# Kernel optimization log

Hardware: AMD Instinct MI355X
Metric: run time of the kernel (lower is better)

The kernel has to match this reference:

```python
import jax, jax.numpy as jnp
import numpy as np

N = 100000        # nodes
E_RAND = 1500000  # random edges (self loops appended -> E = 1.6M)
IN_DIM = 500
HID = 256
NCLASS = 50
K = 10


def setup_inputs() -> dict:
    key = jax.random.key(0)
    ks = jax.random.split(key, 8)
    feats = jax.random.normal(ks[0], (N, IN_DIM), dtype=jnp.float32)
    # edges: random + self loops (fit() adds self loops)
    src_r = jax.random.randint(ks[1], (E_RAND,), 0, N, dtype=jnp.int32)
    dst_r = jax.random.randint(ks[2], (E_RAND,), 0, N, dtype=jnp.int32)
    loop = jnp.arange(N, dtype=jnp.int32)
    src = jnp.concatenate([src_r, loop])
    dst = jnp.concatenate([dst_r, loop])
    # params (xavier-uniform-like scales)
    def xavier(k, shape):
        lim = np.sqrt(6.0 / (shape[0] + shape[1]))
        return jax.random.uniform(k, shape, jnp.float32, -lim, lim)
    W1 = xavier(ks[3], (IN_DIM, HID))
    b1 = jnp.zeros((HID,), jnp.float32)
    W2 = xavier(ks[4], (HID, NCLASS))
    b2 = jnp.zeros((NCLASS,), jnp.float32)
    s = xavier(ks[5], (NCLASS, 1))
    return {"feats": feats, "W1": W1, "b1": b1, "W2": W2, "b2": b2,
            "s": s, "src": src, "dst": dst}


def reference(feats, W1, b1, W2, b2, s, src, dst):
    # --- MLP (dropout is identity in eval / p=0) ---
    x = jax.nn.relu(feats @ W1 + b1)          # [N, HID]
    x = x @ W2 + b2                            # [N, NCLASS]
    # --- DAGNNConv: k-hop sym-normalized propagation ---
    deg = jax.ops.segment_sum(jnp.ones_like(dst, dtype=jnp.float32), dst,
                              num_segments=N)  # in-degrees
    norm = jnp.power(deg, -0.5)[:, None]       # [N, 1]
    results = [x]
    h = x
    for _ in range(K):
        h = h * norm
        h = jax.ops.segment_sum(h[src], dst, num_segments=N)  # copy_u + sum
        h = h * norm
        results.append(h)
    H = jnp.stack(results, axis=1)             # [N, K+1, C]
    S = jax.nn.sigmoid(jnp.einsum('nkc,co->nk', H, s))  # [N, K+1]
    out = jnp.einsum('nk,nkc->nc', S, H)       # [N, C]
    return out
```

## Files before the change

### kernel.cpp

```cpp
#include <hip/hip_runtime.h>
#include <hip/hip_bf16.h>
#include <math.h>

#define NN     100000
#define INDIM  500
#define HID    256
#define NCLASS 50
#define KHOPS  10
#define KPAD   512
#define CPAD   64

static inline size_t roundup256(size_t x) { return (x + 255) & ~(size_t)255; }

typedef __attribute__((ext_vector_type(8))) short bf16x8;
typedef __attribute__((ext_vector_type(4))) float f32x4;
typedef __attribute__((ext_vector_type(4))) short short4v;

__device__ inline short f2bf(float f) {
    union { float f; unsigned u; } v; v.f = f;
    unsigned r = v.u + 0x7FFFu + ((v.u >> 16) & 1u);
    return (short)(r >> 16);
}
__device__ inline float bflo(unsigned u) {
    union { unsigned u; float f; } v; v.u = u << 16; return v.f;
}
__device__ inline float bfhi(unsigned u) {
    union { unsigned u; float f; } v; v.u = u & 0xFFFF0000u; return v.f;
}
__device__ inline unsigned packbf(float a, float b) {
    return (unsigned)(unsigned short)f2bf(a) | ((unsigned)(unsigned short)f2bf(b) << 16);
}

__global__ void dagnn_zero2(int* __restrict__ a, int* __restrict__ b, int n) {
    int i = blockIdx.x * blockDim.x + threadIdx.x;
    if (i < n) { a[i] = 0; b[i] = 0; }
}

__global__ void dagnn_deg(const int* __restrict__ dst, int* __restrict__ degi, int E) {
    int e = blockIdx.x * blockDim.x + threadIdx.x;
    if (e < E) atomicAdd(&degi[dst[e]], 1);
}

__global__ void dagnn_norm(const int* __restrict__ degi, float* __restrict__ nrm, int n) {
    int i = blockIdx.x * blockDim.x + threadIdx.x;
    if (i < n) nrm[i] = rsqrtf((float)degi[i]);
}

__global__ void dagnn_scan(const int* __restrict__ degi, int* __restrict__ rowptr, int n) {
    __shared__ int wsum[16];
    __shared__ int carry_s;
    const int tid  = threadIdx.x;
    const int lane = tid & 63;
    const int wid  = tid >> 6;
    if (tid == 0) carry_s = 0;
    __syncthreads();
    for (int base = 0; base < n; base += 4096) {
        int i0 = base + tid * 4;
        int v0 = (i0 + 0 < n) ? degi[i0 + 0] : 0;
        int v1 = (i0 + 1 < n) ? degi[i0 + 1] : 0;
        int v2 = (i0 + 2 < n) ? degi[i0 + 2] : 0;
        int v3 = (i0 + 3 < n) ? degi[i0 + 3] : 0;
        int tsum = v0 + v1 + v2 + v3;
        int x = tsum;
        #pragma unroll
        for (int off = 1; off < 64; off <<= 1) {
            int t = __shfl_up(x, off);
            if (lane >= off) x += t;
        }
        if (lane == 63) wsum[wid] = x;
        __syncthreads();
        if (tid == 0) {
            int run = carry_s;
            #pragma unroll
            for (int w = 0; w < 16; ++w) { int t = wsum[w]; wsum[w] = run; run += t; }
            carry_s = run;
        }
        __syncthreads();
        int texcl = wsum[wid] + (x - tsum);
        if (i0 + 0 < n) rowptr[i0 + 0] = texcl;
        if (i0 + 1 < n) rowptr[i0 + 1] = texcl + v0;
        if (i0 + 2 < n) rowptr[i0 + 2] = texcl + v0 + v1;
        if (i0 + 3 < n) rowptr[i0 + 3] = texcl + v0 + v1 + v2;
        __syncthreads();
    }
    if (tid == 0) rowptr[n] = carry_s;
}

__global__ void dagnn_fill(const int* __restrict__ src, const int* __restrict__ dst,
                           const int* __restrict__ rowptr, int* __restrict__ fillc,
                           int* __restrict__ colidx, int E) {
    int e = blockIdx.x * blockDim.x + threadIdx.x;
    if (e >= E) return;
    int d = dst[e];
    int pos = rowptr[d] + atomicAdd(&fillc[d], 1);
    colidx[pos] = src[e];
}

__global__ void dagnn_w1t(const float* __restrict__ W1, short* __restrict__ W1t) {
    int idx = blockIdx.x * 256 + threadIdx.x;
    if (idx >= HID * KPAD) return;
    int n = idx >> 9;
    int k = idx & (KPAD - 1);
    float v = (k < INDIM) ? W1[(size_t)k * HID + n] : 0.f;
    W1t[idx] = f2bf(v);
}

__global__ void dagnn_w2t(const float* __restrict__ W2, short* __restrict__ W2t) {
    int idx = blockIdx.x * 256 + threadIdx.x;
    if (idx >= CPAD * HID) return;
    int n = idx >> 8;
    int k = idx & 255;
    float v = (n < NCLASS) ? W2[(size_t)k * NCLASS + n] : 0.f;
    W2t[idx] = f2bf(v);
}

__global__ void dagnn_sgate(const float* __restrict__ svec, float2* __restrict__ sg) {
    int c = threadIdx.x;
    if (c < 32) {
        float x = (2 * c     < NCLASS) ? svec[2 * c]     : 0.f;
        float y = (2 * c + 1 < NCLASS) ? svec[2 * c + 1] : 0.f;
        sg[c] = make_float2(x, y);
    }
}

#define G1_STRIDE 40
__global__ __launch_bounds__(512) void dagnn_gemm1_mfma(
        const float* __restrict__ A, const short* __restrict__ Bt,
        const float* __restrict__ bias, short* __restrict__ C, int M) {
    __shared__ __align__(16) short As[128 * G1_STRIDE];
    __shared__ __align__(16) short Bs[256 * G1_STRIDE];

    const int tid  = threadIdx.x;
    const int lane = tid & 63;
    const int wid  = tid >> 6;
    const int l16  = lane & 15;
    const int quad = lane >> 4;
    const int m_off = (wid & 1) * 64;
    const int n_off = (wid >> 1) * 64;
    const int row0  = blockIdx.x * 128;

    int am[2], aseg[2], bn[2], bseg[2];
    #pragma unroll
    for (int it = 0; it < 2; ++it) {
        int slot = tid + it * 512;
        am[it] = slot >> 3; aseg[it] = slot & 7;
        bn[it] = slot >> 2; bseg[it] = slot & 3;
    }

    float4 ra[2]; bf16x8 rb[2];

    #define LOAD_TILE(k0)                                                     \
        _Pragma("unroll")                                                     \
        for (int it = 0; it < 2; ++it) {                                      \
            int gm = row0 + am[it];                                           \
            int gk = (k0) + aseg[it] * 4;                                     \
            float4 f = {0.f, 0.f, 0.f, 0.f};                                  \
            if (gm < M) {                                                     \
                const float* ap = A + (size_t)gm * INDIM + gk;                \
                if (gk + 3 < INDIM) f = *(const float4*)ap;                   \
                else {                                                        \
                    if (gk + 0 < INDIM) f.x = ap[0];                          \
                    if (gk + 1 < INDIM) f.y = ap[1];                          \
                    if (gk + 2 < INDIM) f.z = ap[2];                          \
                    if (gk + 3 < INDIM) f.w = ap[3];                          \
                }                                                             \
            }                                                                 \
            ra[it] = f;                                                       \
            rb[it] = *(const bf16x8*)(Bt + (size_t)bn[it] * KPAD + (k0) + bseg[it] * 8); \
        }

    #define STORE_TILE()                                                      \
        _Pragma("unroll")                                                     \
        for (int it = 0; it < 2; ++it) {                                      \
            short4v sv;                                                       \
            sv.x = f2bf(ra[it].x); sv.y = f2bf(ra[it].y);                     \
            sv.z = f2bf(ra[it].z); sv.w = f2bf(ra[it].w);                     \
            *(short4v*)&As[am[it] * G1_STRIDE + aseg[it] * 4] = sv;           \
            *(bf16x8*)&Bs[bn[it] * G1_STRIDE + bseg[it] * 8] = rb[it];        \
        }

    f32x4 acc[4][4] = {};

    LOAD_TILE(0)
    STORE_TILE()
    __syncthreads();

    for (int ks = 0; ks < KPAD / 32; ++ks) {
        if (ks + 1 < KPAD / 32) { LOAD_TILE((ks + 1) * 32) }

        bf16x8 af[4], bfr[4];
        #pragma unroll
        for (int mt = 0; mt < 4; ++mt)
            af[mt] = *(const bf16x8*)&As[(m_off + mt * 16 + l16) * G1_STRIDE + quad * 8];
        #pragma unroll
        for (int nt = 0; nt < 4; ++nt)
            bfr[nt] = *(const bf16x8*)&Bs[(n_off + nt * 16 + l16) * G1_STRIDE + quad * 8];
        #pragma unroll
        for (int mt = 0; mt < 4; ++mt)
            #pragma unroll
            for (int nt = 0; nt < 4; ++nt)
                acc[mt][nt] = __builtin_amdgcn_mfma_f32_16x16x32_bf16(
                                  af[mt], bfr[nt], acc[mt][nt], 0, 0, 0);
        __syncthreads();
        if (ks + 1 < KPAD / 32) { STORE_TILE() }
        __syncthreads();
    }
    #undef LOAD_TILE
    #undef STORE_TILE

    #pragma unroll
    for (int nt = 0; nt < 4; ++nt) {
        int gc = n_off + nt * 16 + l16;
        float bb = bias[gc];
        #pragma unroll
        for (int mt = 0; mt < 4; ++mt) {
            #pragma unroll
            for (int r = 0; r < 4; ++r) {
                int gm = row0 + m_off + mt * 16 + quad * 4 + r;
                if (gm < M) {
                    float v = acc[mt][nt][r] + bb;
                    C[(size_t)gm * HID + gc] = f2bf(v > 0.f ? v : 0.f);
                }
            }
        }
    }
}

#define A2_STRIDE 72
#define B2_STRIDE 264
__global__ __launch_bounds__(256) void dagnn_mlp2_mfma(
        const short* __restrict__ hid, const short* __restrict__ W2t,
        const float* __restrict__ b2, const float* __restrict__ svec,
        const float* __restrict__ nrm,
        unsigned* __restrict__ hs0, float* __restrict__ out, int M) {
    __shared__ __align__(16) short As[128 * A2_STRIDE];
    __shared__ __align__(16) short Bs[CPAD * B2_STRIDE];

    const int tid  = threadIdx.x;
    const int lane = tid & 63;
    const int wid  = tid >> 6;
    const int l16  = lane & 15;
    const int quad = lane >> 4;
    const int m_off = wid * 32;
    const int row0  = blockIdx.x * 128;

    #pragma unroll
    for (int it = 0; it < 8; ++it) {
        int slot = tid + it * 256;
        int n   = slot >> 5;
        int seg = slot & 31;
        bf16x8 b = *(const bf16x8*)(W2t + (size_t)n * HID + seg * 8);
        *(bf16x8*)&Bs[n * B2_STRIDE + seg * 8] = b;
    }

    f32x4 acc[2][4] = {};

    for (int ks = 0; ks < HID / 64; ++ks) {
        const int k0 = ks * 64;
        #pragma unroll
        for (int it = 0; it < 4; ++it) {
            int slot = tid + it * 256;
            int m   = slot >> 3;
            int seg = slot & 7;
            int gm  = row0 + m;
            bf16x8 v = {};
            if (gm < M) v = *(const bf16x8*)(hid + (size_t)gm * HID + k0 + seg * 8);
            *(bf16x8*)&As[m * A2_STRIDE + seg * 8] = v;
        }
        __syncthreads();

        #pragma unroll
        for (int ksub = 0; ksub < 2; ++ksub) {
            bf16x8 af[2], bfr[4];
            #pragma unroll
            for (int mt = 0; mt < 2; ++mt)
                af[mt] = *(const bf16x8*)&As[(m_off + mt * 16 + l16) * A2_STRIDE
                                             + ksub * 32 + quad * 8];
            #pragma unroll
            for (int nt = 0; nt < 4; ++nt)
                bfr[nt] = *(const bf16x8*)&Bs[(nt * 16 + l16) * B2_STRIDE
                                              + k0 + ksub * 32 + quad * 8];
            #pragma unroll
            for (int mt = 0; mt < 2; ++mt)
                #pragma unroll
                for (int nt = 0; nt < 4; ++nt)
                    acc[mt][nt] = __builtin_amdgcn_mfma_f32_16x16x32_bf16(
                                      af[mt], bfr[nt], acc[mt][nt], 0, 0, 0);
        }
        __syncthreads();
    }

    float b2v[4], ssv[4];
    #pragma unroll
    for (int nt = 0; nt < 4; ++nt) {
        int gc = nt * 16 + l16;
        b2v[nt] = (gc < NCLASS) ? b2[gc]   : 0.f;
        ssv[nt] = (gc < NCLASS) ? svec[gc] : 0.f;
    }
    #pragma unroll
    for (int mt = 0; mt < 2; ++mt) {
        #pragma unroll
        for (int r = 0; r < 4; ++r) {
            int gm = row0 + m_off + mt * 16 + quad * 4 + r;
            float xv[4], q = 0.f;
            #pragma unroll
            for (int nt = 0; nt < 4; ++nt) {
                xv[nt] = acc[mt][nt][r] + b2v[nt];
                q += xv[nt] * ssv[nt];
            }
            #pragma unroll
            for (int off = 1; off < 16; off <<= 1) q += __shfl_xor(q, off);
            float S = 1.f / (1.f + __expf(-q));
            float nd = (gm < M) ? nrm[gm] : 0.f;
            #pragma unroll
            for (int nt = 0; nt < 4; ++nt) {
                int gc = nt * 16 + l16;
                float hv = xv[nt] * nd;
                float hp = __shfl_xor(hv, 1);
                if (gm < M) {
                    if (!(l16 & 1))
                        hs0[(size_t)gm * 32 + nt * 8 + (l16 >> 1)] = packbf(hv, hp);
                    if (gc < NCLASS) out[(size_t)gm * NCLASS + gc] = S * xv[nt];
                }
            }
        }
    }
}

__global__ __launch_bounds__(256) void dagnn_prop4(
        const unsigned* __restrict__ hs, const float* __restrict__ nrm,
        const int* __restrict__ rowptr, const int* __restrict__ colidx,
        const float2* __restrict__ sgate, unsigned* __restrict__ hs_next,
        float* __restrict__ out, int M, int write_next) {
    const int lane = threadIdx.x & 63;
    const int wid  = threadIdx.x >> 6;
    const int d    = blockIdx.x * 4 + wid;
    if (d >= M) return;
    const int half = lane >> 5;
    const int c    = lane & 31;
    const int beg = rowptr[d], end = rowptr[d + 1];

    float a0 = 0.f, a1 = 0.f;
    int e = beg;
    for (; e + 8 <= end; e += 8) {
        int s0 = colidx[e + half + 0];
        int s1 = colidx[e + half + 2];
        int s2 = colidx[e + half + 4];
        int s3 = colidx[e + half + 6];
        unsigned u0 = hs[(size_t)s0 * 32 + c];
        unsigned u1 = hs[(size_t)s1 * 32 + c];
        unsigned u2 = hs[(size_t)s2 * 32 + c];
        unsigned u3 = hs[(size_t)s3 * 32 + c];
        a0 += (bflo(u0) + bflo(u1)) + (bflo(u2) + bflo(u3));
        a1 += (bfhi(u0) + bfhi(u1)) + (bfhi(u2) + bfhi(u3));
    }
    for (; e + 2 <= end; e += 2) {
        int s = colidx[e + half];
        unsigned u = hs[(size_t)s * 32 + c];
        a0 += bflo(u); a1 += bfhi(u);
    }
    if (e < end && half == 0) {
        int s = colidx[e];
        unsigned u = hs[(size_t)s * 32 + c];
        a0 += bflo(u); a1 += bfhi(u);
    }
    a0 += __shfl_xor(a0, 32);
    a1 += __shfl_xor(a1, 32);

    float nd = nrm[d];
    float r0 = a0 * nd, r1 = a1 * nd;
    float2 g = sgate[c];
    float p = r0 * g.x + r1 * g.y;
    #pragma unroll
    for (int off = 16; off; off >>= 1) p += __shfl_xor(p, off);
    float S = 1.f / (1.f + __expf(-p));
    if (half == 0) {
        if (write_next) hs_next[(size_t)d * 32 + c] = packbf(r0 * nd, r1 * nd);
        int ch = 2 * c;
        if (ch < NCLASS) {
            out[(size_t)d * NCLASS + ch]     += S * r0;
            out[(size_t)d * NCLASS + ch + 1] += S * r1;
        }
    }
}

extern "C" void kernel_launch(void* const* d_in, const int* in_sizes, int n_in,
                              void* d_out, int out_size, void* d_ws, size_t ws_size,
                              hipStream_t stream) {
    const float* feats = (const float*)d_in[0];
    const float* W1    = (const float*)d_in[1];
    const float* b1    = (const float*)d_in[2];
    const float* W2    = (const float*)d_in[3];
    const float* b2    = (const float*)d_in[4];
    const float* svec  = (const float*)d_in[5];
    const int*   src   = (const int*)d_in[6];
    const int*   dst   = (const int*)d_in[7];
    float* out = (float*)d_out;

    const int M = in_sizes[0] / INDIM;
    const int E = in_sizes[6];

    char* p = (char*)d_ws;
    size_t off = 0;
    short*    hid   = (short*)   (p + off); off += roundup256((size_t)M * HID * 2);
    unsigned* hsA   = (unsigned*)(p + off); off += roundup256((size_t)M * 32 * 4);
    unsigned* hsB   = (unsigned*)(p + off); off += roundup256((size_t)M * 32 * 4);
    short*    W1t   = (short*)   (p + off); off += roundup256((size_t)HID * KPAD * 2);
    short*    W2t   = (short*)   (p + off); off += roundup256((size_t)CPAD * HID * 2);
    float2*   sgate = (float2*)  (p + off); off += roundup256(32 * sizeof(float2));
    int*      degi  = (int*)     (p + off); off += roundup256((size_t)M * 4);
    float*    nrm   = (float*)   (p + off); off += roundup256((size_t)M * 4);
    int*      rowptr= (int*)     (p + off); off += roundup256((size_t)(M + 1) * 4);
    int*      fillc = (int*)     (p + off); off += roundup256((size_t)M * 4);
    int*      colidx= (int*)     (p + off); off += roundup256((size_t)E * 4);
    (void)ws_size;

    dagnn_zero2<<<(M + 255) / 256, 256, 0, stream>>>(degi, fillc, M);
    dagnn_deg<<<(E + 255) / 256, 256, 0, stream>>>(dst, degi, E);
    dagnn_norm<<<(M + 255) / 256, 256, 0, stream>>>(degi, nrm, M);
    dagnn_scan<<<1, 1024, 0, stream>>>(degi, rowptr, M);
    dagnn_fill<<<(E + 255) / 256, 256, 0, stream>>>(src, dst, rowptr, fillc, colidx, E);

    dagnn_w1t<<<(HID * KPAD + 255) / 256, 256, 0, stream>>>(W1, W1t);
    dagnn_w2t<<<(CPAD * HID + 255) / 256, 256, 0, stream>>>(W2, W2t);
    dagnn_sgate<<<1, 32, 0, stream>>>(svec, sgate);

    dagnn_gemm1_mfma<<<(M + 127) / 128, 512, 0, stream>>>(feats, W1t, b1, hid, M);
    dagnn_mlp2_mfma<<<(M + 127) / 128, 256, 0, stream>>>(hid, W2t, b2, svec, nrm,
                                                         hsA, out, M);

    unsigned* hin = hsA;
    unsigned* hout = hsB;
    for (int k = 0; k < KHOPS; ++k) {
        dagnn_prop4<<<(M + 3) / 4, 256, 0, stream>>>(hin, nrm, rowptr, colidx,
                                                     sgate, hout, out, M,
                                                     k < KHOPS - 1);
        unsigned* t = hin; hin = hout; hout = t;
    }
}
```

Baseline: 1.168 ms.

## Use direct global-to-LDS loads in GEMM1 and warp-shuffled edge indices in propagation

GEMM1 now loads fp32 feature tiles and a pre-tiled bf16 W1 straight into double-buffered, XOR-swizzled LDS with global_load_lds. The bf16 conversion moves to fragment load time, and the output goes through an LDS-staged, vectorised epilogue. This is meant to remove the register round trip and one barrier per k-step, at the cost of much larger LDS use (66 KB), which limits blocks per CU. The propagation kernel now loads up to 64 column indices per wave once and broadcasts them with shuffles, and it prefetches the output accumulator early to hide gather latency.

```diff
diff --git a/kernel.cpp b/kernel.cpp
--- a/kernel.cpp
+++ b/kernel.cpp
@@ -16,10 +16,17 @@
 typedef __attribute__((ext_vector_type(4))) float f32x4;
 typedef __attribute__((ext_vector_type(4))) short short4v;
 
+typedef __attribute__((address_space(3))) unsigned       lds_u32;
+typedef const __attribute__((address_space(1))) unsigned glb_u32;
+
 __device__ inline short f2bf(float f) {
     union { float f; unsigned u; } v; v.f = f;
     unsigned r = v.u + 0x7FFFu + ((v.u >> 16) & 1u);
     return (short)(r >> 16);
+}
+__device__ inline short f2bf_hw(float f) {
+    __hip_bfloat16 h = __float2bfloat16(f);
+    return *reinterpret_cast<short*>(&h);
 }
 __device__ inline float bflo(unsigned u) {
     union { unsigned u; float f; } v; v.u = u << 16; return v.f;
@@ -96,13 +103,15 @@
     colidx[pos] = src[e];
 }
 
-__global__ void dagnn_w1t(const float* __restrict__ W1, short* __restrict__ W1t) {
+__global__ void dagnn_w1ts(const float* __restrict__ W1, short* __restrict__ Bts) {
     int idx = blockIdx.x * 256 + threadIdx.x;
     if (idx >= HID * KPAD) return;
-    int n = idx >> 9;
-    int k = idx & (KPAD - 1);
+    int ks = idx >> 13;
+    int n  = (idx >> 5) & 255;
+    int kk = idx & 31;
+    int k  = ks * 32 + kk;
     float v = (k < INDIM) ? W1[(size_t)k * HID + n] : 0.f;
-    W1t[idx] = f2bf(v);
+    Bts[idx] = f2bf(v);
 }
 
 __global__ void dagnn_w2t(const float* __restrict__ W2, short* __restrict__ W2t) {
@@ -123,12 +132,35 @@
     }
 }
 
-#define G1_STRIDE 40
-__global__ __launch_bounds__(512) void dagnn_gemm1_mfma(
-        const float* __restrict__ A, const short* __restrict__ Bt,
+#define G1_STAGE(ABASE, BBASE, KS)                                             \
+    {                                                                          \
+        const int k0_ = (KS) * 32;                                             \
+        _Pragma("unroll")                                                      \
+        for (int j = 0; j < 2; ++j) {                                          \
+            int slot = (wid * 2 + j) * 64 + lane;                              \
+            int mrow = slot >> 3;                                  \
+            int q    = (slot & 7) ^ (mrow & 7);    \
+            int gm   = row0 + mrow;                                            \
+            int gk   = k0_ + q * 4;                                            \
+            const float* asrc = (gm < M && gk < INDIM)                         \
+                ? (A + (size_t)gm * INDIM + gk) : A;                           \
+            __builtin_amdgcn_global_load_lds((glb_u32*)asrc,                   \
+                (lds_u32*)((ABASE) + (wid * 2 + j) * 256), 16, 0, 0);          \
+            const short* bsrc = Bts + ((size_t)(KS) << 13) + slot * 8;         \
+            __builtin_amdgcn_global_load_lds((glb_u32*)bsrc,                   \
+                (lds_u32*)((BBASE) + (wid * 2 + j) * 512), 16, 0, 0);          \
+        }                                                                      \
+    }
+
+__global__ __launch_bounds__(512, 4) void dagnn_gemm1_mfma(
+        const float* __restrict__ A, const short* __restrict__ Bts,
         const float* __restrict__ bias, short* __restrict__ C, int M) {
-    __shared__ __align__(16) short As[128 * G1_STRIDE];
-    __shared__ __align__(16) short Bs[256 * G1_STRIDE];
+    __shared__ __align__(16) char smem[67584];
+    float* As0 = (float*)smem;
+    float* As1 = (float*)(smem + 16384);
+    short* Bs0 = (short*)(smem + 32768);
+    short* Bs1 = (short*)(smem + 49152);
+    short* Ep  = (short*)smem;
 
     const int tid  = threadIdx.x;
     const int lane = tid & 63;
@@ -139,90 +171,76 @@
     const int n_off = (wid >> 1) * 64;
     const int row0  = blockIdx.x * 128;
 
-    int am[2], aseg[2], bn[2], bseg[2];
-    #pragma unroll
-    for (int it = 0; it < 2; ++it) {
-        int slot = tid + it * 512;
-        am[it] = slot >> 3; aseg[it] = slot & 7;
-        bn[it] = slot >> 2; bseg[it] = slot & 3;
-    }
-
-    float4 ra[2]; bf16x8 rb[2];
-
-    #define LOAD_TILE(k0)                                                     \
-        _Pragma("unroll")                                                     \
-        for (int it = 0; it < 2; ++it) {                                      \
-            int gm = row0 + am[it];                                           \
-            int gk = (k0) + aseg[it] * 4;                                     \
-            float4 f = {0.f, 0.f, 0.f, 0.f};                                  \
-            if (gm < M) {                                                     \
-                const float* ap = A + (size_t)gm * INDIM + gk;                \
-                if (gk + 3 < INDIM) f = *(const float4*)ap;                   \
-                else {                                                        \
-                    if (gk + 0 < INDIM) f.x = ap[0];                          \
-                    if (gk + 1 < INDIM) f.y = ap[1];                          \
-                    if (gk + 2 < INDIM) f.z = ap[2];                          \
-                    if (gk + 3 < INDIM) f.w = ap[3];                          \
-                }                                                             \
-            }                                                                 \
-            ra[it] = f;                                                       \
-            rb[it] = *(const bf16x8*)(Bt + (size_t)bn[it] * KPAD + (k0) + bseg[it] * 8); \
-        }
-
-    #define STORE_TILE()                                                      \
-        _Pragma("unroll")                                                     \
-        for (int it = 0; it < 2; ++it) {                                      \
-            short4v sv;                                                       \
-            sv.x = f2bf(ra[it].x); sv.y = f2bf(ra[it].y);                     \
-            sv.z = f2bf(ra[it].z); sv.w = f2bf(ra[it].w);                     \
-            *(short4v*)&As[am[it] * G1_STRIDE + aseg[it] * 4] = sv;           \
-            *(bf16x8*)&Bs[bn[it] * G1_STRIDE + bseg[it] * 8] = rb[it];        \
-        }
-
     f32x4 acc[4][4] = {};
 
-    LOAD_TILE(0)
-    STORE_TILE()
+    G1_STAGE(As0, Bs0, 0)
     __syncthreads();
 
     for (int ks = 0; ks < KPAD / 32; ++ks) {
-        if (ks + 1 < KPAD / 32) { LOAD_TILE((ks + 1) * 32) }
-
-        bf16x8 af[4], bfr[4];
-        #pragma unroll
-        for (int mt = 0; mt < 4; ++mt)
-            af[mt] = *(const bf16x8*)&As[(m_off + mt * 16 + l16) * G1_STRIDE + quad * 8];
+        const int cur = ks & 1;
+        const float* ab = cur ? As1 : As0;
+        const short* bb = cur ? Bs1 : Bs0;
+        if (ks + 1 < KPAD / 32) {
+            if (cur) { G1_STAGE(As0, Bs0, ks + 1) }
+            else     { G1_STAGE(As1, Bs1, ks + 1) }
+        }
+
+        bf16x8 bfr[4];
         #pragma unroll
         for (int nt = 0; nt < 4; ++nt)
-            bfr[nt] = *(const bf16x8*)&Bs[(n_off + nt * 16 + l16) * G1_STRIDE + quad * 8];
-        #pragma unroll
-        for (int mt = 0; mt < 4; ++mt)
+            bfr[nt] = *(const bf16x8*)(bb + (n_off + nt * 16 + l16) * 32 + quad * 8);
+
+        #pragma unroll
+        for (int mt = 0; mt < 4; ++mt) {
+            int m  = m_off + mt * 16 + l16;
+            int s0 = (quad * 2 + 0) ^ (m & 7);
+            int s1 = (quad * 2 + 1) ^ (m & 7);
+            float4 lo = *(const float4*)(ab + m * 32 + s0 * 4);
+            float4 hi = *(const float4*)(ab + m * 32 + s1 * 4);
+            bf16x8 af;
+            af[0] = f2bf_hw(lo.x); af[1] = f2bf_hw(lo.y);
+            af[2] = f2bf_hw(lo.z); af[3] = f2bf_hw(lo.w);
+            af[4] = f2bf_hw(hi.x); af[5] = f2bf_hw(hi.y);
+            af[6] = f2bf_hw(hi.z); af[7] = f2bf_hw(hi.w);
             #pragma unroll
             for (int nt = 0; nt < 4; ++nt)
                 acc[mt][nt] = __builtin_amdgcn_mfma_f32_16x16x32_bf16(
-                                  af[mt], bfr[nt], acc[mt][nt], 0, 0, 0);
-        __syncthreads();
-        if (ks + 1 < KPAD / 32) { STORE_TILE() }
-        __syncthreads();
-    }
-    #undef LOAD_TILE
-    #undef STORE_TILE
-
-    #pragma unroll
-    for (int nt = 0; nt < 4; ++nt) {
-        int gc = n_off + nt * 16 + l16;
-        float bb = bias[gc];
-        #pragma unroll
-        for (int mt = 0; mt < 4; ++mt) {
+                                  af, bfr[nt], acc[mt][nt], 0, 0, 0);
+        }
+        __syncthreads();
+    }
+
+    float bv[4];
+    #pragma unroll
+    for (int nt = 0; nt < 4; ++nt) bv[nt] = bias[n_off + nt * 16 + l16];
+
+    #pragma unroll
+    for (int mt = 0; mt < 4; ++mt) {
+        #pragma unroll
+        for (int nt = 0; nt < 4; ++nt) {
             #pragma unroll
             for (int r = 0; r < 4; ++r) {
-                int gm = row0 + m_off + mt * 16 + quad * 4 + r;
-                if (gm < M) {
-                    float v = acc[mt][nt][r] + bb;
-                    C[(size_t)gm * HID + gc] = f2bf(v > 0.f ? v : 0.f);
+                float v = acc[mt][nt][r] + bv[nt];
+                v = v > 0.f ? v : 0.f;
+                float vp = __shfl_xor(v, 1);
+                if (!(l16 & 1)) {
+                    int mrel = m_off + mt * 16 + quad * 4 + r;
+                    *(unsigned*)(Ep + mrel * 264 + n_off + nt * 16 + l16) =
+                        packbf(v, vp);
                 }
             }
         }
+    }
+    __syncthreads();
+    #pragma unroll
+    for (int it = 0; it < 8; ++it) {
+        int cidx = tid + it * 512;
+        int rr   = cidx >> 5;
+        int chk  = cidx & 31;
+        int gm   = row0 + rr;
+        if (gm < M)
+            *(bf16x8*)(C + (size_t)gm * HID + chk * 8) =
+                *(const bf16x8*)(Ep + rr * 264 + chk * 8);
     }
 }
 
@@ -327,7 +345,7 @@
     }
 }
 
-__global__ __launch_bounds__(256) void dagnn_prop4(
+__global__ __launch_bounds__(256) void dagnn_prop5(
         const unsigned* __restrict__ hs, const float* __restrict__ nrm,
         const int* __restrict__ rowptr, const int* __restrict__ colidx,
         const float2* __restrict__ sgate, unsigned* __restrict__ hs_next,
@@ -339,35 +357,46 @@
     const int half = lane >> 5;
     const int c    = lane & 31;
     const int beg = rowptr[d], end = rowptr[d + 1];
+    const int deg = end - beg;
+    const float nd = nrm[d];
+
+    const int ch = 2 * c;
+    float o0 = 0.f, o1 = 0.f;
+    const bool ow = (half == 0) && (ch < NCLASS);
+    if (ow) {
+        o0 = out[(size_t)d * NCLASS + ch];
+        o1 = out[(size_t)d * NCLASS + ch + 1];
+    }
+
+    int cv = (lane < deg) ? colidx[beg + lane] : 0;
 
     float a0 = 0.f, a1 = 0.f;
-    int e = beg;
-    for (; e + 8 <= end; e += 8) {
-        int s0 = colidx[e + half + 0];
-        int s1 = colidx[e + half + 2];
-        int s2 = colidx[e + half + 4];
-        int s3 = colidx[e + half + 6];
-        unsigned u0 = hs[(size_t)s0 * 32 + c];
-        unsigned u1 = hs[(size_t)s1 * 32 + c];
-        unsigned u2 = hs[(size_t)s2 * 32 + c];
-        unsigned u3 = hs[(size_t)s3 * 32 + c];
-        a0 += (bflo(u0) + bflo(u1)) + (bflo(u2) + bflo(u3));
-        a1 += (bfhi(u0) + bfhi(u1)) + (bfhi(u2) + bfhi(u3));
-    }
-    for (; e + 2 <= end; e += 2) {
+    const int dmain = deg > 64 ? 64 : deg;
+    for (int i = 0; i < dmain; i += 16) {
+        #pragma unroll
+        for (int t = 0; t < 8; ++t) {
+            int ei = i + half * 8 + t;
+            int s = __shfl(cv, ei);
+            if (ei < dmain) {
+                unsigned u = hs[(size_t)s * 32 + c];
+                a0 += bflo(u); a1 += bfhi(u);
+            }
+        }
+    }
+    for (int e = beg + 64; e + 2 <= end; e += 2) {
         int s = colidx[e + half];
         unsigned u = hs[(size_t)s * 32 + c];
         a0 += bflo(u); a1 += bfhi(u);
     }
-    if (e < end && half == 0) {
-        int s = colidx[e];
+    if (deg > 64 && ((deg - 64) & 1) && half == 0) {
+        int s = colidx[end - 1];
         unsigned u = hs[(size_t)s * 32 + c];
         a0 += bflo(u); a1 += bfhi(u);
     }
+
     a0 += __shfl_xor(a0, 32);
     a1 += __shfl_xor(a1, 32);
 
-    float nd = nrm[d];
     float r0 = a0 * nd, r1 = a1 * nd;
     float2 g = sgate[c];
     float p = r0 * g.x + r1 * g.y;
@@ -376,10 +405,9 @@
     float S = 1.f / (1.f + __expf(-p));
     if (half == 0) {
         if (write_next) hs_next[(size_t)d * 32 + c] = packbf(r0 * nd, r1 * nd);
-        int ch = 2 * c;
         if (ch < NCLASS) {
-            out[(size_t)d * NCLASS + ch]     += S * r0;
-            out[(size_t)d * NCLASS + ch + 1] += S * r1;
+            out[(size_t)d * NCLASS + ch]     = o0 + S * r0;
+            out[(size_t)d * NCLASS + ch + 1] = o1 + S * r1;
         }
     }
 }
@@ -421,7 +449,7 @@
     dagnn_scan<<<1, 1024, 0, stream>>>(degi, rowptr, M);
     dagnn_fill<<<(E + 255) / 256, 256, 0, stream>>>(src, dst, rowptr, fillc, colidx, E);
 
-    dagnn_w1t<<<(HID * KPAD + 255) / 256, 256, 0, stream>>>(W1, W1t);
+    dagnn_w1ts<<<(HID * KPAD + 255) / 256, 256, 0, stream>>>(W1, W1t);
     dagnn_w2t<<<(CPAD * HID + 255) / 256, 256, 0, stream>>>(W2, W2t);
     dagnn_sgate<<<1, 32, 0, stream>>>(svec, sgate);
 
@@ -432,7 +460,7 @@
     unsigned* hin = hsA;
     unsigned* hout = hsB;
     for (int k = 0; k < KHOPS; ++k) {
-        dagnn_prop4<<<(M + 3) / 4, 256, 0, stream>>>(hin, nrm, rowptr, colidx,
+        dagnn_prop5<<<(M + 3) / 4, 256, 0, stream>>>(hin, nrm, rowptr, colidx,
                                                      sgate, hout, out, M,
                                                      k < KHOPS - 1);
         unsigned* t = hin; hin = hout; hout = t;
```

Result: slower. 1.287 ms (+10.1%).
